# Performance work log

Measured on AMD Instinct MI355X. Metric: run time of the kernel, lower is better.

## Reference

```python
import jax, jax.numpy as jnp
import numpy as np

VOCAB = 50000
EMBED = 512
HIDDEN = 1024
HDIR = HIDDEN // 2  # per-direction LSTM hidden
L = 48              # num_labels
B = 64
T = 512
PAD = 0


def setup_inputs() -> dict:
    key = jax.random.key(0)
    ks = jax.random.split(key, 18)
    def n(k, shape, s=0.05):
        return jax.random.normal(k, shape, jnp.float32) * s
    return {
        "embedding": n(ks[0], (VOCAB, EMBED)),
        "w_ih_f": n(ks[1], (4 * HDIR, EMBED)),
        "w_hh_f": n(ks[2], (4 * HDIR, HDIR)),
        "b_ih_f": n(ks[3], (4 * HDIR,)),
        "b_hh_f": n(ks[4], (4 * HDIR,)),
        "w_ih_b": n(ks[5], (4 * HDIR, EMBED)),
        "w_hh_b": n(ks[6], (4 * HDIR, HDIR)),
        "b_ih_b": n(ks[7], (4 * HDIR,)),
        "b_hh_b": n(ks[8], (4 * HDIR,)),
        "fc_w": n(ks[9], (L, HIDDEN)),
        "fc_b": n(ks[10], (L,)),
        "start_trans": n(ks[11], (L,), 0.1),
        "end_trans": n(ks[12], (L,), 0.1),
        "trans": n(ks[13], (L, L), 0.1),
        "x": jax.random.randint(ks[14], (B, T), 1, VOCAB),   # >=1 so mask all-true
        "tags": jax.random.randint(ks[15], (B, T), 0, L),
    }


def _lstm_dir(emb_tbe, w_ih, w_hh, b_ih, b_hh, reverse):
    # emb_tbe: [T, B, E] -> hs: [T, B, HDIR]; PyTorch gate order i,f,g,o
    Hd = w_hh.shape[1]
    Bb = emb_tbe.shape[1]
    bias = b_ih + b_hh
    def step(carry, x_t):
        h, c = carry
        g = x_t @ w_ih.T + h @ w_hh.T + bias
        i, f, gg, o = jnp.split(g, 4, axis=-1)
        c = jax.nn.sigmoid(f) * c + jax.nn.sigmoid(i) * jnp.tanh(gg)
        h = jax.nn.sigmoid(o) * jnp.tanh(c)
        return (h, c), h
    init = (jnp.zeros((Bb, Hd), emb_tbe.dtype), jnp.zeros((Bb, Hd), emb_tbe.dtype))
    _, hs = jax.lax.scan(step, init, emb_tbe, reverse=reverse)
    return hs


def _crf_nll(emissions_tbl, maskf_tb, tags, start_trans, end_trans, trans):
    # emissions_tbl: [T, B, L]; maskf_tb: [T, B] float; tags: [B, T] int
    em_bt = emissions_tbl.transpose(1, 0, 2)                           # [B, T, L]
    em_tag = jnp.take_along_axis(em_bt, tags[..., None], -1)[..., 0]   # [B, T]
    tr = trans[tags[:, :-1], tags[:, 1:]]                              # [B, T-1]
    mask_bt = maskf_tb.T                                               # [B, T]
    num = start_trans[tags[:, 0]] + em_tag[:, 0] \
        + jnp.sum((em_tag[:, 1:] + tr) * mask_bt[:, 1:], axis=1)
    last_idx = (mask_bt.sum(axis=1) - 1).astype(jnp.int32)
    last_tags = jnp.take_along_axis(tags, last_idx[:, None], 1)[:, 0]
    num = num + end_trans[last_tags]
    # forward algorithm (log partition)
    alpha0 = start_trans[None, :] + emissions_tbl[0]                   # [B, L]
    def step(alpha, inp):
        e_t, m_t = inp
        new = jax.nn.logsumexp(alpha[:, :, None] + trans[None, :, :] + e_t[:, None, :], axis=1)
        return jnp.where(m_t[:, None] > 0, new, alpha), None
    alpha, _ = jax.lax.scan(step, alpha0, (emissions_tbl[1:], maskf_tb[1:]))
    logZ = jax.nn.logsumexp(alpha + end_trans[None, :], axis=-1)       # [B]
    llh = num - logZ
    return -jnp.mean(llh)  # reduction='mean' over batch, negated


def reference(embedding, w_ih_f, w_hh_f, b_ih_f, b_hh_f,
              w_ih_b, w_hh_b, b_ih_b, b_hh_b,
              fc_w, fc_b, start_trans, end_trans, trans, x, tags):
    mask = (x != PAD)                                  # [B, T]
    emb = embedding[x]                                 # [B, T, E]
    emb_t = emb.transpose(1, 0, 2)                     # [T, B, E]
    hf = _lstm_dir(emb_t, w_ih_f, w_hh_f, b_ih_f, b_hh_f, reverse=False)
    hb = _lstm_dir(emb_t, w_ih_b, w_hh_b, b_ih_b, b_hh_b, reverse=True)
    h = jnp.concatenate([hf, hb], axis=-1)             # [T, B, HIDDEN]
    emissions = h @ fc_w.T + fc_b                      # [T, B, L]
    maskf = mask.T.astype(emissions.dtype)             # [T, B]
    return _crf_nll(emissions, maskf, tags, start_trans, end_trans, trans)
```

## Files before the change

### kernel.cpp

```cpp
#include <hip/hip_runtime.h>
#include <hip/hip_bf16.h>


typedef short short8  __attribute__((ext_vector_type(8)));
typedef short short4v __attribute__((ext_vector_type(4)));
typedef float floatx4 __attribute__((ext_vector_type(4)));

#define OFF_XQ    0ULL
#define OFF_H     268435456ULL
#define OFF_EMB   335544320ULL
#define OFF_WIH   369098752ULL
#define OFF_FCW   373293056ULL
#define OFF_BIAS  373391360ULL
#define OFF_EM    373538816ULL
#define OFF_NUM   379830272ULL
#define OFF_LOGZ  379830528ULL
#define WS_NEED   379830784ULL

__device__ __forceinline__ unsigned short f2bf(float f) {
  __hip_bfloat16 h = __float2bfloat16(f);
  unsigned short u; __builtin_memcpy(&u, &h, 2); return u;
}
__device__ __forceinline__ float bf2f(unsigned short u) {
  __hip_bfloat16 h; __builtin_memcpy(&h, &u, 2); return __bfloat162float(h);
}
__device__ __forceinline__ float sigm(float x) { return 1.0f / (1.0f + __expf(-x)); }
__device__ __forceinline__ float tanh_f(float x) {
  x = fmaxf(fminf(x, 15.0f), -15.0f);
  float e = __expf(2.0f * x);
  return (e - 1.0f) / (e + 1.0f);
}
__device__ __forceinline__ int permt(int t) { return (t * 167) & 511; }

__global__ void k_init(uint4* __restrict__ H) {
  size_t i = (size_t)blockIdx.x * 256 + threadIdx.x;
  H[i] = (uint4){0xFFFFFFFFu, 0xFFFFFFFFu, 0xFFFFFFFFu, 0xFFFFFFFFu};
}

__global__ void k0_conv(const float* __restrict__ wf, const float* __restrict__ wb,
                        const float* __restrict__ fcw,
                        const float* __restrict__ bihf, const float* __restrict__ bhhf,
                        const float* __restrict__ bihb, const float* __restrict__ bhhb,
                        unsigned short* __restrict__ wih_bf,
                        unsigned short* __restrict__ fcw_bf,
                        float* __restrict__ bias) {
  int i = blockIdx.x * 256 + threadIdx.x;
  if (i < 1048576) { wih_bf[i] = f2bf(wf[i]); return; }
  int j = i - 1048576;
  if (j < 1048576) { wih_bf[1048576 + j] = f2bf(wb[j]); return; }
  j -= 1048576;
  if (j < 49152) { fcw_bf[j] = f2bf(fcw[j]); return; }
  j -= 49152;
  if (j < 2048) { bias[j] = bihf[j] + bhhf[j]; return; }
  j -= 2048;
  if (j < 2048) { bias[2048 + j] = bihb[j] + bhhb[j]; return; }
}

__global__ void k1_embed(const float* __restrict__ tab, const int* __restrict__ x,
                         unsigned short* __restrict__ emb_bf) {
  int tid = threadIdx.x;
#pragma unroll
  for (int r = 0; r < 4; ++r) {
    int m = blockIdx.x * 4 + r;
    int b = m & 63, t = m >> 6;
    int tok = x[b * 512 + t];
    const float2* src = (const float2*)(tab + (size_t)tok * 512);
    float2 v = src[tid];
    unsigned int pk = (unsigned int)f2bf(v.x) | ((unsigned int)f2bf(v.y) << 16);
    ((unsigned int*)(emb_bf + (size_t)m * 512))[tid] = pk;
  }
}

__global__ __launch_bounds__(256) void k2_xproj(
    const unsigned short* __restrict__ emb_bf, const unsigned short* __restrict__ wih_bf,
    const float* __restrict__ bias, unsigned short* __restrict__ xq) {
  const int mt = blockIdx.x * 128;
  const int nt = blockIdx.y * 128;
  const int d  = blockIdx.z;
  const unsigned short* W = wih_bf + (size_t)d * 2048 * 512;
  __shared__ short Bs[32768];
  const int tid = threadIdx.x, l = tid & 63, wv = tid >> 6;
  const int mh = wv & 1, nh = wv >> 1;
  floatx4 acc[4][4];
#pragma unroll
  for (int a = 0; a < 4; ++a)
#pragma unroll
    for (int b = 0; b < 4; ++b) acc[a][b] = (floatx4){0.f, 0.f, 0.f, 0.f};
  const unsigned short* Abase = emb_bf + (size_t)(mt + mh * 64) * 512;

  for (int kc = 0; kc < 2; ++kc) {
    __syncthreads();
#pragma unroll
    for (int i = 0; i < 16; ++i) {
      int f = i * 4 + wv;
      int nb2 = f & 7, ks = f >> 3;
      int n = nt + nb2 * 16 + (l & 15);
      int k = kc * 256 + ks * 32 + (l >> 4) * 8;
      short8 v = *(const short8*)(W + (size_t)n * 512 + k);
      *(short8*)(Bs + (f * 64 + l) * 8) = v;
    }
    __syncthreads();
#pragma unroll
    for (int ks = 0; ks < 8; ++ks) {
      int k0 = kc * 256 + ks * 32 + (l >> 4) * 8;
      short8 a[4];
#pragma unroll
      for (int mf = 0; mf < 4; ++mf)
        a[mf] = *(const short8*)(Abase + (size_t)(mf * 16 + (l & 15)) * 512 + k0);
#pragma unroll
      for (int nf = 0; nf < 4; ++nf) {
        short8 bfr = *(const short8*)(Bs + ((ks * 8 + nh * 4 + nf) * 64 + l) * 8);
#pragma unroll
        for (int mf = 0; mf < 4; ++mf)
          acc[mf][nf] = __builtin_amdgcn_mfma_f32_16x16x32_bf16(a[mf], bfr, acc[mf][nf], 0, 0, 0);
      }
    }
  }
  __syncthreads();
#pragma unroll
  for (int nf = 0; nf < 4; ++nf) {
    int nl = nh * 64 + nf * 16 + (l & 15);
    float bs = bias[d * 2048 + nt + nl];
#pragma unroll
    for (int mf = 0; mf < 4; ++mf)
#pragma unroll
      for (int r = 0; r < 4; ++r) {
        int ml = mh * 64 + mf * 16 + (l >> 4) * 4 + r;
        Bs[ml * 136 + nl] = (short)f2bf(acc[mf][nf][r] + bs);
      }
  }
  __syncthreads();
  const int chunk = tid >> 3, sub = tid & 7;
  const int g_l = chunk & 15, t_l = chunk >> 4;
  const int gate = nt >> 9, g0 = (nt & 511) >> 3;
  size_t base = (((size_t)(d * 64 + g0 + g_l) * 512) + (size_t)(blockIdx.x * 2 + t_l)) * 2048
                + (size_t)gate * 512 + (size_t)sub * 64;
#pragma unroll
  for (int i = 0; i < 8; ++i) {
    short8 v = *(const short8*)(Bs + (t_l * 64 + sub * 8 + i) * 136 + g_l * 8);
    *(short8*)(xq + base + i * 8) = v;
  }
}

__global__ __launch_bounds__(256, 1) void k3_lstm(
    const float* __restrict__ whh_f, const float* __restrict__ whh_b,
    const unsigned short* __restrict__ xq, unsigned short* __restrict__ Hall) {
  const int wgid = blockIdx.x;
  const int d = wgid >> 6, g = wgid & 63;
  const int tid = threadIdx.x, l = tid & 63, wv = tid >> 6;
  const float* whh = d ? whh_b : whh_f;

  short8 Bf[32];
#pragma unroll
  for (int ks = 0; ks < 16; ++ks) {
#pragma unroll
    for (int nf = 0; nf < 2; ++nf) {
      int nl = nf * 16 + (l & 15);
      int gate = nl >> 3, cell = nl & 7;
      int row = gate * 512 + g * 8 + cell;
      int k0 = ks * 32 + (l >> 4) * 8;
      const float* src = whh + (size_t)row * 512 + k0;
      short8 v;
#pragma unroll
      for (int j = 0; j < 8; ++j) v[j] = (short)f2bf(src[j]);
      Bf[ks * 2 + nf] = v;
    }
  }

  __shared__ float gsh2[2][32][66];
  const int i6 = tid & 63, q = tid >> 6;
  const int eb = q * 16 + (i6 >> 2);
  const int pr = tid & 3;
  float cst[2] = {0.f, 0.f};

  const unsigned short* Hd = Hall + (size_t)d * 16777216;
  unsigned int* Hw = (unsigned int*)Hall + (size_t)d * 8388608;
  const unsigned short* xqd = xq + ((size_t)(d * 64 + g) * 512) * 2048;

  const int st_idx = (q * 16 + (g >> 2)) * 256 + 64 * (g & 3) + i6;

  for (int s = 0; s < 512; ++s) {
    const int t = d ? (511 - s) : s;

    const unsigned int* xb = (const unsigned int*)(xqd + (size_t)t * 2048);
    unsigned int xg[4];
#pragma unroll
    for (int gate = 0; gate < 4; ++gate) xg[gate] = xb[gate * 256 + tid];

    floatx4 acc0 = (floatx4){0.f, 0.f, 0.f, 0.f};
    floatx4 acc1 = (floatx4){0.f, 0.f, 0.f, 0.f};
    if (s > 0) {
      const int tp = d ? (t + 1) : (t - 1);
      const unsigned long long* Hu =
          (const unsigned long long*)(Hd + (size_t)permt(tp) * 32768 + (size_t)wv * 8192);
      unsigned long long u[32];
      for (;;) {
#pragma unroll
        for (int ks = 0; ks < 16; ++ks) {
          u[2 * ks]     = __hip_atomic_load(Hu + (size_t)ks * 128 + l * 2,
                                            __ATOMIC_RELAXED, __HIP_MEMORY_SCOPE_AGENT);
          u[2 * ks + 1] = __hip_atomic_load(Hu + (size_t)ks * 128 + l * 2 + 1,
                                            __ATOMIC_RELAXED, __HIP_MEMORY_SCOPE_AGENT);
        }
        bool ok = true;
#pragma unroll
        for (int i = 0; i < 32; ++i) {
          ok &= ((unsigned int)u[i] != 0xFFFFFFFFu);
          ok &= ((unsigned int)(u[i] >> 32) != 0xFFFFFFFFu);
        }
        if (__all((int)ok)) break;
        __builtin_amdgcn_s_sleep(1);
      }
#pragma unroll
      for (int ks = 0; ks < 16; ++ks) {
        short8 af;
        __builtin_memcpy(&af, &u[2 * ks], 8);
        __builtin_memcpy(((char*)&af) + 8, &u[2 * ks + 1], 8);
        acc0 = __builtin_amdgcn_mfma_f32_16x16x32_bf16(af, Bf[ks * 2 + 0], acc0, 0, 0, 0);
        acc1 = __builtin_amdgcn_mfma_f32_16x16x32_bf16(af, Bf[ks * 2 + 1], acc1, 0, 0, 0);
      }
    }
    const int sb = s & 1;
#pragma unroll
    for (int r = 0; r < 4; ++r) {
      int m = wv * 16 + (l >> 4) * 4 + r;
      gsh2[sb][l & 15][m] = acc0[r];
      gsh2[sb][16 + (l & 15)][m] = acc1[r];
    }
    __syncthreads();
    float h2[2];
#pragma unroll
    for (int ci = 0; ci < 2; ++ci) {
      int cl = pr * 2 + ci;
      float gi = gsh2[sb][0 + cl][eb]  + bf2f((unsigned short)(xg[0] >> (ci * 16)));
      float gf = gsh2[sb][8 + cl][eb]  + bf2f((unsigned short)(xg[1] >> (ci * 16)));
      float gg = gsh2[sb][16 + cl][eb] + bf2f((unsigned short)(xg[2] >> (ci * 16)));
      float go = gsh2[sb][24 + cl][eb] + bf2f((unsigned short)(xg[3] >> (ci * 16)));
      float c = sigm(gf) * cst[ci] + sigm(gi) * tanh_f(gg);
      cst[ci] = c;
      h2[ci] = sigm(go) * tanh_f(c);
    }
    unsigned int hp = (unsigned int)f2bf(h2[0]) | ((unsigned int)f2bf(h2[1]) << 16);
    __hip_atomic_store(&Hw[(size_t)permt(t) * 16384 + st_idx], hp,
                       __ATOMIC_RELAXED, __HIP_MEMORY_SCOPE_AGENT);
  }
}

__global__ __launch_bounds__(256) void k4_emis(
    const unsigned short* __restrict__ Hall, const unsigned short* __restrict__ fcw_bf,
    const float* __restrict__ fcb, float* __restrict__ em) {
  __shared__ short Fs[48 * 520];
  const int tid = threadIdx.x, l = tid & 63, wv = tid >> 6;
  const int t = blockIdx.x;
  floatx4 acc[3];
  acc[0] = acc[1] = acc[2] = (floatx4){0.f, 0.f, 0.f, 0.f};
  for (int half = 0; half < 2; ++half) {
    __syncthreads();
#pragma unroll
    for (int i = 0; i < 24; ++i) {
      int e4 = (tid + i * 256) * 4;
      int n = e4 >> 9, k = e4 & 511;
      *(short4v*)(Fs + n * 520 + k) =
          *(const short4v*)(fcw_bf + (size_t)n * 1024 + half * 512 + k);
    }
    __syncthreads();
    const unsigned short* Hsrc = Hall + (size_t)half * 16777216 + (size_t)permt(t) * 32768
                                 + (size_t)wv * 8192 + l * 8;
#pragma unroll
    for (int ks = 0; ks < 16; ++ks) {
      short8 a = *(const short8*)(Hsrc + ks * 512);
#pragma unroll
      for (int nf = 0; nf < 3; ++nf) {
        short8 bfr = *(const short8*)(Fs + (nf * 16 + (l & 15)) * 520 + ks * 32 + (l >> 4) * 8);
        acc[nf] = __builtin_amdgcn_mfma_f32_16x16x32_bf16(a, bfr, acc[nf], 0, 0, 0);
      }
    }
  }
#pragma unroll
  for (int nf = 0; nf < 3; ++nf) {
    int n = nf * 16 + (l & 15);
    float bv = fcb[n];
#pragma unroll
    for (int r = 0; r < 4; ++r) {
      int m = wv * 16 + (l >> 4) * 4 + r;
      em[((size_t)t * 64 + m) * 48 + n] = acc[nf][r] + bv;
    }
  }
}

__global__ void k5_num(const float* __restrict__ em, const int* __restrict__ tags,
                       const float* __restrict__ start, const float* __restrict__ endt,
                       const float* __restrict__ trans, float* __restrict__ num) {
  const int b = blockIdx.x, tid = threadIdx.x;
  float s = 0.f;
  for (int t = 1 + tid; t < 512; t += 256) {
    int tg = tags[b * 512 + t], tp = tags[b * 512 + t - 1];
    s += em[(size_t)(t * 64 + b) * 48 + tg] + trans[tp * 48 + tg];
  }
  if (tid == 0) {
    int t0 = tags[b * 512];
    s += start[t0] + em[(size_t)b * 48 + t0] + endt[tags[b * 512 + 511]];
  }
  __shared__ float red[256];
  red[tid] = s;
  __syncthreads();
  for (int o = 128; o > 0; o >>= 1) {
    if (tid < o) red[tid] += red[tid + o];
    __syncthreads();
  }
  if (tid == 0) num[b] = red[0];
}

__global__ void k6_crf(const float* __restrict__ em, const float* __restrict__ trans,
                       const float* __restrict__ start, const float* __restrict__ endt,
                       float* __restrict__ logz) {
  const int b = blockIdx.x;
  const int j = threadIdx.x;
  const bool act = j < 48;
  float Ecol[48];
#pragma unroll
  for (int i = 0; i < 48; ++i) Ecol[i] = act ? __expf(trans[i * 48 + j]) : 0.f;
  __shared__ float p[48];
  float alpha = act ? (start[j] + em[(size_t)b * 48 + j]) : -1e30f;
  for (int t = 1; t < 512; ++t) {
    float e_t = act ? em[(size_t)(t * 64 + b) * 48 + j] : 0.f;
    float m = alpha;
#pragma unroll
    for (int off = 32; off > 0; off >>= 1) m = fmaxf(m, __shfl_xor(m, off));
    if (act) p[j] = __expf(alpha - m);
    float ssum = 0.f;
#pragma unroll
    for (int i = 0; i < 48; ++i) ssum += p[i] * Ecol[i];
    alpha = act ? (m + __logf(ssum) + e_t) : -1e30f;
  }
  float v = act ? (alpha + endt[j]) : -1e30f;
  float m2 = v;
#pragma unroll
  for (int off = 32; off > 0; off >>= 1) m2 = fmaxf(m2, __shfl_xor(m2, off));
  float sz = act ? __expf(v - m2) : 0.f;
#pragma unroll
  for (int off = 32; off > 0; off >>= 1) sz += __shfl_xor(sz, off);
  if (j == 0) logz[b] = m2 + __logf(sz);
}

__global__ void k7_final(const float* __restrict__ num, const float* __restrict__ logz,
                         float* __restrict__ out) {
  int l = threadIdx.x;
  float v = num[l] - logz[l];
#pragma unroll
  for (int off = 32; off > 0; off >>= 1) v += __shfl_xor(v, off);
  if (l == 0) out[0] = -v * (1.0f / 64.0f);
}

extern "C" void kernel_launch(void* const* d_in, const int* in_sizes, int n_in,
                              void* d_out, int out_size, void* d_ws, size_t ws_size,
                              hipStream_t stream) {
  (void)in_sizes; (void)n_in; (void)out_size;
  if (ws_size < WS_NEED) return;

  const float* embedding = (const float*)d_in[0];
  const float* w_ih_f = (const float*)d_in[1];
  const float* w_hh_f = (const float*)d_in[2];
  const float* b_ih_f = (const float*)d_in[3];
  const float* b_hh_f = (const float*)d_in[4];
  const float* w_ih_b = (const float*)d_in[5];
  const float* w_hh_b = (const float*)d_in[6];
  const float* b_ih_b = (const float*)d_in[7];
  const float* b_hh_b = (const float*)d_in[8];
  const float* fc_w = (const float*)d_in[9];
  const float* fc_b = (const float*)d_in[10];
  const float* start_trans = (const float*)d_in[11];
  const float* end_trans = (const float*)d_in[12];
  const float* trans = (const float*)d_in[13];
  const int* x = (const int*)d_in[14];
  const int* tags = (const int*)d_in[15];

  char* ws = (char*)d_ws;
  unsigned short* xq     = (unsigned short*)(ws + OFF_XQ);
  unsigned short* Hall   = (unsigned short*)(ws + OFF_H);
  unsigned short* emb_bf = (unsigned short*)(ws + OFF_EMB);
  unsigned short* wih_bf = (unsigned short*)(ws + OFF_WIH);
  unsigned short* fcw_bf = (unsigned short*)(ws + OFF_FCW);
  float* bias  = (float*)(ws + OFF_BIAS);
  float* em    = (float*)(ws + OFF_EM);
  float* num   = (float*)(ws + OFF_NUM);
  float* logz  = (float*)(ws + OFF_LOGZ);

  k_init<<<16384, 256, 0, stream>>>((uint4*)Hall);
  k0_conv<<<8400, 256, 0, stream>>>(w_ih_f, w_ih_b, fc_w, b_ih_f, b_hh_f, b_ih_b, b_hh_b,
                                    wih_bf, fcw_bf, bias);
  k1_embed<<<8192, 256, 0, stream>>>(embedding, x, emb_bf);
  k2_xproj<<<dim3(256, 16, 2), 256, 0, stream>>>(emb_bf, wih_bf, bias, xq);
  k3_lstm<<<128, 256, 0, stream>>>(w_hh_f, w_hh_b, xq, Hall);
  k4_emis<<<512, 256, 0, stream>>>(Hall, fcw_bf, fc_b, em);
  k5_num<<<64, 256, 0, stream>>>(em, tags, start_trans, end_trans, trans, num);
  k6_crf<<<64, 64, 0, stream>>>(em, trans, start_trans, end_trans, logz);
  k7_final<<<1, 64, 0, stream>>>(num, logz, (float*)d_out);
}
```

Baseline: 2.651 ms.

## Remove per-step block barrier by computing LSTM cells in registers with shuffles

The recurrent LSTM step now swaps MFMA operand order so each lane holds gate values for its own batch row. Gates are exchanged with a cross-half-wave shuffle instead of going through shared memory and a __syncthreads. Polling for the previous hidden state becomes per-k-slice: each slice's MFMA runs as soon as its data is ready rather than waiting for all of it. Hidden-state stores become 64-bit writes from half the lanes, with a changed H layout. This targets the per-step latency of the serial recurrence, but adds divergent polling loops and removes the sleep backoff.

```diff
diff --git a/kernel.cpp b/kernel.cpp
--- a/kernel.cpp
+++ b/kernel.cpp
@@ -167,82 +167,90 @@
     }
   }
 
-  __shared__ float gsh2[2][32][66];
-  const int i6 = tid & 63, q = tid >> 6;
-  const int eb = q * 16 + (i6 >> 2);
-  const int pr = tid & 3;
-  float cst[2] = {0.f, 0.f};
-
-  const unsigned short* Hd = Hall + (size_t)d * 16777216;
-  unsigned int* Hw = (unsigned int*)Hall + (size_t)d * 8388608;
+  const int q  = l >> 4;
+  const int bl = l & 15;
+  const int Q  = q & 1;
+  const int b  = wv * 16 + bl;
+  float cst[4] = {0.f, 0.f, 0.f, 0.f};
+
+  const unsigned long long* Hb =
+      (const unsigned long long*)((const unsigned int*)Hall + (size_t)d * 8388608);
+  unsigned long long* Hwb =
+      (unsigned long long*)((unsigned int*)Hall + (size_t)d * 8388608);
   const unsigned short* xqd = xq + ((size_t)(d * 64 + g) * 512) * 2048;
 
-  const int st_idx = (q * 16 + (g >> 2)) * 256 + 64 * (g & 3) + i6;
+  const size_t st8 = (size_t)wv * 2048 + (size_t)(g >> 2) * 128 + (size_t)(g & 3) * 32
+                     + 2 * bl + Q;
 
   for (int s = 0; s < 512; ++s) {
     const int t = d ? (511 - s) : s;
 
-    const unsigned int* xb = (const unsigned int*)(xqd + (size_t)t * 2048);
-    unsigned int xg[4];
-#pragma unroll
-    for (int gate = 0; gate < 4; ++gate) xg[gate] = xb[gate * 256 + tid];
+    const unsigned long long* xb = (const unsigned long long*)(xqd + (size_t)t * 2048);
+    unsigned long long xu[4];
+#pragma unroll
+    for (int gate = 0; gate < 4; ++gate) xu[gate] = xb[gate * 128 + b * 2 + Q];
 
     floatx4 acc0 = (floatx4){0.f, 0.f, 0.f, 0.f};
     floatx4 acc1 = (floatx4){0.f, 0.f, 0.f, 0.f};
     if (s > 0) {
       const int tp = d ? (t + 1) : (t - 1);
-      const unsigned long long* Hu =
-          (const unsigned long long*)(Hd + (size_t)permt(tp) * 32768 + (size_t)wv * 8192);
+      const unsigned long long* Hu = Hb + (size_t)permt(tp) * 8192 + (size_t)wv * 2048;
       unsigned long long u[32];
-      for (;;) {
+#pragma unroll
+      for (int ks = 0; ks < 16; ++ks) {
+        u[2 * ks]     = __hip_atomic_load(Hu + (size_t)ks * 128 + 2 * l,
+                                          __ATOMIC_RELAXED, __HIP_MEMORY_SCOPE_AGENT);
+        u[2 * ks + 1] = __hip_atomic_load(Hu + (size_t)ks * 128 + 2 * l + 1,
+                                          __ATOMIC_RELAXED, __HIP_MEMORY_SCOPE_AGENT);
+      }
+      unsigned ready = 0;
+      while (ready != 0xFFFFu) {
 #pragma unroll
         for (int ks = 0; ks < 16; ++ks) {
-          u[2 * ks]     = __hip_atomic_load(Hu + (size_t)ks * 128 + l * 2,
-                                            __ATOMIC_RELAXED, __HIP_MEMORY_SCOPE_AGENT);
-          u[2 * ks + 1] = __hip_atomic_load(Hu + (size_t)ks * 128 + l * 2 + 1,
-                                            __ATOMIC_RELAXED, __HIP_MEMORY_SCOPE_AGENT);
+          if (!((ready >> ks) & 1u)) {
+            unsigned long long a0 = u[2 * ks], a1 = u[2 * ks + 1];
+            bool ok = ((unsigned)a0 != 0xFFFFFFFFu) && ((unsigned)(a0 >> 32) != 0xFFFFFFFFu)
+                   && ((unsigned)a1 != 0xFFFFFFFFu) && ((unsigned)(a1 >> 32) != 0xFFFFFFFFu);
+            if (__all((int)ok)) {
+              ready |= 1u << ks;
+              short8 af;
+              __builtin_memcpy(&af, &a0, 8);
+              __builtin_memcpy((char*)&af + 8, &a1, 8);
+              acc0 = __builtin_amdgcn_mfma_f32_16x16x32_bf16(Bf[ks * 2 + 0], af, acc0, 0, 0, 0);
+              acc1 = __builtin_amdgcn_mfma_f32_16x16x32_bf16(Bf[ks * 2 + 1], af, acc1, 0, 0, 0);
+            } else {
+              u[2 * ks]     = __hip_atomic_load(Hu + (size_t)ks * 128 + 2 * l,
+                                                __ATOMIC_RELAXED, __HIP_MEMORY_SCOPE_AGENT);
+              u[2 * ks + 1] = __hip_atomic_load(Hu + (size_t)ks * 128 + 2 * l + 1,
+                                                __ATOMIC_RELAXED, __HIP_MEMORY_SCOPE_AGENT);
+            }
+          }
         }
-        bool ok = true;
-#pragma unroll
-        for (int i = 0; i < 32; ++i) {
-          ok &= ((unsigned int)u[i] != 0xFFFFFFFFu);
-          ok &= ((unsigned int)(u[i] >> 32) != 0xFFFFFFFFu);
-        }
-        if (__all((int)ok)) break;
-        __builtin_amdgcn_s_sleep(1);
       }
-#pragma unroll
-      for (int ks = 0; ks < 16; ++ks) {
-        short8 af;
-        __builtin_memcpy(&af, &u[2 * ks], 8);
-        __builtin_memcpy(((char*)&af) + 8, &u[2 * ks + 1], 8);
-        acc0 = __builtin_amdgcn_mfma_f32_16x16x32_bf16(af, Bf[ks * 2 + 0], acc0, 0, 0, 0);
-        acc1 = __builtin_amdgcn_mfma_f32_16x16x32_bf16(af, Bf[ks * 2 + 1], acc1, 0, 0, 0);
-      }
-    }
-    const int sb = s & 1;
+    }
+    float h4[4];
 #pragma unroll
     for (int r = 0; r < 4; ++r) {
-      int m = wv * 16 + (l >> 4) * 4 + r;
-      gsh2[sb][l & 15][m] = acc0[r];
-      gsh2[sb][16 + (l & 15)][m] = acc1[r];
-    }
-    __syncthreads();
-    float h2[2];
-#pragma unroll
-    for (int ci = 0; ci < 2; ++ci) {
-      int cl = pr * 2 + ci;
-      float gi = gsh2[sb][0 + cl][eb]  + bf2f((unsigned short)(xg[0] >> (ci * 16)));
-      float gf = gsh2[sb][8 + cl][eb]  + bf2f((unsigned short)(xg[1] >> (ci * 16)));
-      float gg = gsh2[sb][16 + cl][eb] + bf2f((unsigned short)(xg[2] >> (ci * 16)));
-      float go = gsh2[sb][24 + cl][eb] + bf2f((unsigned short)(xg[3] >> (ci * 16)));
-      float c = sigm(gf) * cst[ci] + sigm(gi) * tanh_f(gg);
-      cst[ci] = c;
-      h2[ci] = sigm(go) * tanh_f(c);
-    }
-    unsigned int hp = (unsigned int)f2bf(h2[0]) | ((unsigned int)f2bf(h2[1]) << 16);
-    __hip_atomic_store(&Hw[(size_t)permt(t) * 16384 + st_idx], hp,
-                       __ATOMIC_RELAXED, __HIP_MEMORY_SCOPE_AGENT);
+      float s0 = __shfl_xor(acc0[r], 32);
+      float s1 = __shfl_xor(acc1[r], 32);
+      float gi = (q < 2) ? acc0[r] : s0;
+      float gf = (q < 2) ? s0 : acc0[r];
+      float gg = (q < 2) ? acc1[r] : s1;
+      float go = (q < 2) ? s1 : acc1[r];
+      gi += bf2f((unsigned short)(xu[0] >> (16 * r)));
+      gf += bf2f((unsigned short)(xu[1] >> (16 * r)));
+      gg += bf2f((unsigned short)(xu[2] >> (16 * r)));
+      go += bf2f((unsigned short)(xu[3] >> (16 * r)));
+      float c = sigm(gf) * cst[r] + sigm(gi) * tanh_f(gg);
+      cst[r] = c;
+      h4[r] = sigm(go) * tanh_f(c);
+    }
+    unsigned int d0 = (unsigned int)f2bf(h4[0]) | ((unsigned int)f2bf(h4[1]) << 16);
+    unsigned int d1 = (unsigned int)f2bf(h4[2]) | ((unsigned int)f2bf(h4[3]) << 16);
+    unsigned long long hp = (unsigned long long)d0 | ((unsigned long long)d1 << 32);
+    if (q < 2)
+      __hip_atomic_store(Hwb + (size_t)permt(t) * 8192 + st8, hp,
+                         __ATOMIC_RELAXED, __HIP_MEMORY_SCOPE_AGENT);
   }
 }
 
```

New measurement: 4.568 ms. 72.3% more time.

## Swap MFMA operands so gates land in registers, removing LDS exchange and barrier

Applied to the files above, without the earlier changes.

The recurrent LSTM kernel now puts the weight fragments in the A operand and the hidden state in B, with the weight rows reordered so one lane's four accumulator values are the i, f, g, o gates of one cell. That removes the shared-memory transpose and the per-step __syncthreads. The 16-step K loop is also split into two independent accumulator chains to shorten MFMA dependency latency. The x-projection indexing and the h store layout change to match, which risks a mismatch with how downstream kernels read H.

```diff
diff --git a/kernel.cpp b/kernel.cpp
--- a/kernel.cpp
+++ b/kernel.cpp
@@ -154,52 +154,54 @@
 #pragma unroll
   for (int ks = 0; ks < 16; ++ks) {
 #pragma unroll
-    for (int nf = 0; nf < 2; ++nf) {
-      int nl = nf * 16 + (l & 15);
-      int gate = nl >> 3, cell = nl & 7;
-      int row = gate * 512 + g * 8 + cell;
+    for (int T = 0; T < 2; ++T) {
+      int nl = l & 15;
+      int cA = nl >> 2, gate = nl & 3;
+      int row = gate * 512 + g * 8 + 2 * cA + T;
       int k0 = ks * 32 + (l >> 4) * 8;
       const float* src = whh + (size_t)row * 512 + k0;
       short8 v;
 #pragma unroll
       for (int j = 0; j < 8; ++j) v[j] = (short)f2bf(src[j]);
-      Bf[ks * 2 + nf] = v;
-    }
-  }
-
-  __shared__ float gsh2[2][32][66];
-  const int i6 = tid & 63, q = tid >> 6;
-  const int eb = q * 16 + (i6 >> 2);
-  const int pr = tid & 3;
+      Bf[ks * 2 + T] = v;
+    }
+  }
+
+  const int q  = l >> 4;
+  const int bl = l & 15;
+  const int m  = wv * 16 + bl;
   float cst[2] = {0.f, 0.f};
 
-  const unsigned short* Hd = Hall + (size_t)d * 16777216;
+  const unsigned long long* Hb =
+      (const unsigned long long*)((const unsigned int*)Hall + (size_t)d * 8388608);
   unsigned int* Hw = (unsigned int*)Hall + (size_t)d * 8388608;
   const unsigned short* xqd = xq + ((size_t)(d * 64 + g) * 512) * 2048;
 
-  const int st_idx = (q * 16 + (g >> 2)) * 256 + 64 * (g & 3) + i6;
+  const size_t st_dw = (size_t)wv * 4096 + (size_t)(g >> 2) * 256
+                     + (size_t)(g & 3) * 64 + bl * 4 + q;
 
   for (int s = 0; s < 512; ++s) {
     const int t = d ? (511 - s) : s;
 
     const unsigned int* xb = (const unsigned int*)(xqd + (size_t)t * 2048);
-    unsigned int xg[4];
-#pragma unroll
-    for (int gate = 0; gate < 4; ++gate) xg[gate] = xb[gate * 256 + tid];
-
-    floatx4 acc0 = (floatx4){0.f, 0.f, 0.f, 0.f};
-    floatx4 acc1 = (floatx4){0.f, 0.f, 0.f, 0.f};
+    unsigned int xu[4];
+#pragma unroll
+    for (int gate = 0; gate < 4; ++gate) xu[gate] = xb[gate * 256 + m * 4 + q];
+
+    floatx4 acc0  = (floatx4){0.f, 0.f, 0.f, 0.f};
+    floatx4 acc1  = (floatx4){0.f, 0.f, 0.f, 0.f};
+    floatx4 acc0b = (floatx4){0.f, 0.f, 0.f, 0.f};
+    floatx4 acc1b = (floatx4){0.f, 0.f, 0.f, 0.f};
     if (s > 0) {
       const int tp = d ? (t + 1) : (t - 1);
-      const unsigned long long* Hu =
-          (const unsigned long long*)(Hd + (size_t)permt(tp) * 32768 + (size_t)wv * 8192);
+      const unsigned long long* Hu = Hb + (size_t)permt(tp) * 8192 + (size_t)wv * 2048;
       unsigned long long u[32];
       for (;;) {
 #pragma unroll
         for (int ks = 0; ks < 16; ++ks) {
-          u[2 * ks]     = __hip_atomic_load(Hu + (size_t)ks * 128 + l * 2,
+          u[2 * ks]     = __hip_atomic_load(Hu + (size_t)ks * 128 + 2 * l,
                                             __ATOMIC_RELAXED, __HIP_MEMORY_SCOPE_AGENT);
-          u[2 * ks + 1] = __hip_atomic_load(Hu + (size_t)ks * 128 + l * 2 + 1,
+          u[2 * ks + 1] = __hip_atomic_load(Hu + (size_t)ks * 128 + 2 * l + 1,
                                             __ATOMIC_RELAXED, __HIP_MEMORY_SCOPE_AGENT);
         }
         bool ok = true;
@@ -212,36 +214,35 @@
         __builtin_amdgcn_s_sleep(1);
       }
 #pragma unroll
-      for (int ks = 0; ks < 16; ++ks) {
-        short8 af;
-        __builtin_memcpy(&af, &u[2 * ks], 8);
-        __builtin_memcpy(((char*)&af) + 8, &u[2 * ks + 1], 8);
-        acc0 = __builtin_amdgcn_mfma_f32_16x16x32_bf16(af, Bf[ks * 2 + 0], acc0, 0, 0, 0);
-        acc1 = __builtin_amdgcn_mfma_f32_16x16x32_bf16(af, Bf[ks * 2 + 1], acc1, 0, 0, 0);
+      for (int ks = 0; ks < 8; ++ks) {
+        short8 af0, af1;
+        __builtin_memcpy(&af0, &u[2 * ks], 8);
+        __builtin_memcpy((char*)&af0 + 8, &u[2 * ks + 1], 8);
+        __builtin_memcpy(&af1, &u[2 * (ks + 8)], 8);
+        __builtin_memcpy((char*)&af1 + 8, &u[2 * (ks + 8) + 1], 8);
+        acc0  = __builtin_amdgcn_mfma_f32_16x16x32_bf16(Bf[ks * 2 + 0], af0, acc0, 0, 0, 0);
+        acc1  = __builtin_amdgcn_mfma_f32_16x16x32_bf16(Bf[ks * 2 + 1], af0, acc1, 0, 0, 0);
+        acc0b = __builtin_amdgcn_mfma_f32_16x16x32_bf16(Bf[(ks + 8) * 2 + 0], af1, acc0b, 0, 0, 0);
+        acc1b = __builtin_amdgcn_mfma_f32_16x16x32_bf16(Bf[(ks + 8) * 2 + 1], af1, acc1b, 0, 0, 0);
       }
-    }
-    const int sb = s & 1;
-#pragma unroll
-    for (int r = 0; r < 4; ++r) {
-      int m = wv * 16 + (l >> 4) * 4 + r;
-      gsh2[sb][l & 15][m] = acc0[r];
-      gsh2[sb][16 + (l & 15)][m] = acc1[r];
-    }
-    __syncthreads();
+      acc0 += acc0b;
+      acc1 += acc1b;
+    }
+
     float h2[2];
 #pragma unroll
-    for (int ci = 0; ci < 2; ++ci) {
-      int cl = pr * 2 + ci;
-      float gi = gsh2[sb][0 + cl][eb]  + bf2f((unsigned short)(xg[0] >> (ci * 16)));
-      float gf = gsh2[sb][8 + cl][eb]  + bf2f((unsigned short)(xg[1] >> (ci * 16)));
-      float gg = gsh2[sb][16 + cl][eb] + bf2f((unsigned short)(xg[2] >> (ci * 16)));
-      float go = gsh2[sb][24 + cl][eb] + bf2f((unsigned short)(xg[3] >> (ci * 16)));
-      float c = sigm(gf) * cst[ci] + sigm(gi) * tanh_f(gg);
-      cst[ci] = c;
-      h2[ci] = sigm(go) * tanh_f(c);
+    for (int T = 0; T < 2; ++T) {
+      floatx4 a = T ? acc1 : acc0;
+      float gi = a[0] + bf2f((unsigned short)(xu[0] >> (16 * T)));
+      float gf = a[1] + bf2f((unsigned short)(xu[1] >> (16 * T)));
+      float gg = a[2] + bf2f((unsigned short)(xu[2] >> (16 * T)));
+      float go = a[3] + bf2f((unsigned short)(xu[3] >> (16 * T)));
+      float c = sigm(gf) * cst[T] + sigm(gi) * tanh_f(gg);
+      cst[T] = c;
+      h2[T] = sigm(go) * tanh_f(c);
     }
     unsigned int hp = (unsigned int)f2bf(h2[0]) | ((unsigned int)f2bf(h2[1]) << 16);
-    __hip_atomic_store(&Hw[(size_t)permt(t) * 16384 + st_idx], hp,
+    __hip_atomic_store(&Hw[(size_t)permt(t) * 16384 + st_dw], hp,
                        __ATOMIC_RELAXED, __HIP_MEMORY_SCOPE_AGENT);
   }
 }
```

Measured after the change: 2.873 ms. 8.4% more time.
